# Optimization experiments

Hardware: AMD Instinct MI355X
Metric: run time of the kernel (lower is better)

Reference implementation:

```python
import jax, jax.numpy as jnp
import numpy as np

EPS = 1e-6          # module eps for denominator
KERNEL_EPS = 1e-4   # performer softmax_kernel numerical eps


def softmax_kernel(data, projection):
    # data: [n, l, h, e]; projection: [m, e] -> features [n, l, h, m]
    d = data.shape[-1]
    m = projection.shape[0]
    data_normalizer = d ** -0.25
    ratio = m ** -0.5
    data_dash = jnp.einsum('nlhe,me->nlhm', data * data_normalizer, projection)
    diag_data = (0.5 * (data_normalizer ** 2)) * jnp.sum(data * data, axis=-1, keepdims=True)
    # numerically stable exp with per-row max subtraction
    data_dash = ratio * (jnp.exp(data_dash - diag_data - jnp.max(data_dash, axis=-1, keepdims=True)) + KERNEL_EPS)
    return data_dash


def _gaussian_orthogonal_random_matrix(nb_rows, nb_cols, seed=0):
    rng = np.random.default_rng(seed)
    blocks = []
    for _ in range(int(np.ceil(nb_rows / nb_cols))):
        q, _ = np.linalg.qr(rng.standard_normal((nb_cols, nb_cols)))
        blocks.append(q.T)
    proj = np.concatenate(blocks, axis=0)[:nb_rows]
    # scaling=0: chi-distributed row multipliers
    multiplier = np.linalg.norm(rng.standard_normal((nb_rows, nb_cols)), axis=1)
    return (multiplier[:, None] * proj).astype(np.float32)


def setup_inputs() -> dict:
    n, l, h, e = 2, 2048, 8, 64
    nb_features = l  # module: nb_features = l when l >= e
    key = jax.random.key(0)
    kq, kk, kv = jax.random.split(key, 3)
    queries = jax.random.normal(kq, (n, l, h, e), jnp.float32)
    keys = jax.random.normal(kk, (n, l, h, e), jnp.float32)
    values = jax.random.normal(kv, (n, l, h, e), jnp.float32)
    projection = jnp.asarray(_gaussian_orthogonal_random_matrix(nb_features, e))
    return {"queries": queries, "keys": keys, "values": values, "projection": projection}


def reference(queries, keys, values, projection):
    # Performer linear attention, batched (bi=None) branch
    q = softmax_kernel(queries, projection)   # [n, l, h, m]
    k = softmax_kernel(keys, projection)      # [n, l, h, m]
    kv = jnp.einsum('nshm,nshe->nhem', k, values)              # [n, h, e, m]
    z = 1.0 / (jnp.einsum('nlhm,nhm->nlh', q, k.sum(axis=1)) + EPS)  # [n, l, h]
    v = jnp.einsum('nlhm,nhem,nlh->nlhe', q, kv, z)             # [n, l, h, e]
    return v
```

## Files before the change

### kernel.cpp

```cpp
#include <hip/hip_runtime.h>


#define LL 2048
#define HH 8
#define MM 2048
#define ROWSTR 512

#define NORMC 0.35355339059327373f
#define LOG2E 1.4426950408889634f
#define NORMC2 (NORMC * LOG2E)
#define RATIO 0.022097086912079608f
#define KEPS 1e-4f
#define REPS (RATIO * KEPS)
#define EPSD 1e-6f

#define KVSPLIT 2097152
#define RSPLIT 32768

typedef __attribute__((ext_vector_type(8))) short short8;
typedef __attribute__((ext_vector_type(16))) float f32x16;

#define MFMA32(a, b, c) __builtin_amdgcn_mfma_f32_32x32x16_bf16((a), (b), (c), 0, 0, 0)

__device__ __forceinline__ void wg_barrier_lds() {
    asm volatile("s_waitcnt lgkmcnt(0)" ::: "memory");
    __builtin_amdgcn_s_barrier();
    __builtin_amdgcn_sched_barrier(0);
}

__device__ __forceinline__ f32x16 zero16() {
    f32x16 v;
    #pragma unroll
    for (int i = 0; i < 16; ++i) v[i] = 0.f;
    return v;
}
__device__ __forceinline__ unsigned short f2bf(float f) {
    union { float f; unsigned int u; } v; v.f = f;
    unsigned int r = v.u + 0x7fffu + ((v.u >> 16) & 1u);
    return (unsigned short)(r >> 16);
}
__device__ __forceinline__ unsigned int pk2(float lo, float hi) {
    return __builtin_amdgcn_perm(__float_as_uint(hi), __float_as_uint(lo), 0x07060302u);
}
__device__ __forceinline__ float bf2f(unsigned short u) {
    union { unsigned int ui; float f; } v; v.ui = ((unsigned int)u) << 16; return v.f;
}

template <bool BF16>
__device__ __forceinline__ short8 row_load8(const void* src, size_t rowbase, int off) {
    if (BF16) {
        return *(const short8*)((const unsigned short*)src + rowbase + off);
    } else {
        const float* p = (const float*)src + rowbase + off;
        float4 f0 = ((const float4*)p)[0], f1 = ((const float4*)p)[1];
        union { unsigned int u[4]; short8 s; } v;
        v.u[0] = pk2(f0.x, f0.y); v.u[1] = pk2(f0.z, f0.w);
        v.u[2] = pk2(f1.x, f1.y); v.u[3] = pk2(f1.z, f1.w);
        return v.s;
    }
}

template <bool BF16>
__device__ __forceinline__ void tile_load(const void* src, size_t base, size_t rstride,
                                          int t, uint4& A, uint4& B) {
    const int row = t >> 2, c16 = (t & 3) * 16;
    if (BF16) {
        const unsigned short* p = (const unsigned short*)src + base + (size_t)row * rstride + c16;
        A = *(const uint4*)p;
        B = *(const uint4*)(p + 8);
    } else {
        const float* p = (const float*)src + base + (size_t)row * rstride + c16;
        float4 f0 = ((const float4*)p)[0], f1 = ((const float4*)p)[1];
        float4 f2 = ((const float4*)p)[2], f3 = ((const float4*)p)[3];
        A.x = pk2(f0.x, f0.y); A.y = pk2(f0.z, f0.w);
        A.z = pk2(f1.x, f1.y); A.w = pk2(f1.z, f1.w);
        B.x = pk2(f2.x, f2.y); B.y = pk2(f2.z, f2.w);
        B.z = pk2(f3.x, f3.y); B.w = pk2(f3.z, f3.w);
    }
}
__device__ __forceinline__ void tile_store72(unsigned short* D, int t, uint4 A, uint4 B) {
    const int row = t >> 2, c16 = (t & 3) * 16;
    *(uint4*)&D[row * 72 + c16] = A;
    *(uint4*)&D[row * 72 + c16 + 8] = B;
}

template <bool BF16>
__device__ __forceinline__ void vt_load(const void* V, size_t base, int t, uint4& A, uint4& B) {
    const int s0 = (t & 31) * 2, e0 = (t >> 5) * 8;
    if (BF16) {
        const unsigned short* p = (const unsigned short*)V + base + (size_t)s0 * ROWSTR + e0;
        A = *(const uint4*)p;
        B = *(const uint4*)(p + ROWSTR);
    } else {
        const float* p = (const float*)V + base + (size_t)s0 * ROWSTR + e0;
        float4 f0 = ((const float4*)p)[0], f1 = ((const float4*)p)[1];
        const float* q = p + ROWSTR;
        float4 g0 = ((const float4*)q)[0], g1 = ((const float4*)q)[1];
        A.x = pk2(f0.x, f0.y); A.y = pk2(f0.z, f0.w);
        A.z = pk2(f1.x, f1.y); A.w = pk2(f1.z, f1.w);
        B.x = pk2(g0.x, g0.y); B.y = pk2(g0.z, g0.w);
        B.z = pk2(g1.x, g1.y); B.w = pk2(g1.z, g1.w);
    }
}
__device__ __forceinline__ void vt_store72(unsigned short* VT, int t, uint4 A, uint4 B) {
    const int s0 = (t & 31) * 2, e0 = (t >> 5) * 8;
    const unsigned ua[4] = {A.x, A.y, A.z, A.w}, ub[4] = {B.x, B.y, B.z, B.w};
    #pragma unroll
    for (int i = 0; i < 4; ++i) {
        *(unsigned*)&VT[(e0 + 2 * i) * 72 + s0] = (ua[i] & 0xFFFFu) | (ub[i] << 16);
        *(unsigned*)&VT[(e0 + 2 * i + 1) * 72 + s0] = (ua[i] >> 16) | (ub[i] & 0xFFFF0000u);
    }
}

__device__ __forceinline__ short8 xfrag(const unsigned int pd[8], int cp, int hi) {
    const unsigned int s0 = hi ? pd[4 * cp + 0] : pd[4 * cp + 2];
    const unsigned int s1 = hi ? pd[4 * cp + 1] : pd[4 * cp + 3];
    const unsigned int r0 = (unsigned int)__shfl_xor((int)s0, 32);
    const unsigned int r1 = (unsigned int)__shfl_xor((int)s1, 32);
    union { unsigned int u[4]; short8 s; } v;
    v.u[0] = hi ? r0 : pd[4 * cp + 0];
    v.u[1] = hi ? r1 : pd[4 * cp + 1];
    v.u[2] = hi ? pd[4 * cp + 2] : r0;
    v.u[3] = hi ? pd[4 * cp + 3] : r1;
    return v.s;
}

__global__ void LinearAttention_15985868276494_detect(const unsigned short* __restrict__ P,
                                                      float* __restrict__ flag) {
    if (threadIdx.x == 0) {
        int sane = 1;
        #pragma unroll
        for (int i = 0; i < 16; ++i) {
            const unsigned e = (P[2 * i] >> 7) & 0xFF;
            if (e < 101 || e > 141) sane = 0;
        }
        *flag = sane ? 1.0f : 0.0f;
    }
}

template <bool BF16>
__device__ void stats_impl(const void* X, const void* P, float* cws, char* smem) {
    unsigned short* Ps = (unsigned short*)smem;
    float* red = (float*)(smem + 73728);
    const int t = threadIdx.x;
    const int w = t >> 6, ln = t & 31, hi = (t >> 5) & 1;
    const int mstrip = w & 1, r3 = (w >> 1) & 3, tsel = w >> 3;
    const int grp = w >> 2, tl = t & 255;
    const int row_base = blockIdx.x * 128;

    short8 xb[4];
    #pragma unroll
    for (int c = 0; c < 4; ++c)
        xb[c] = row_load8<BF16>(X, (size_t)(row_base + r3 * 32 + ln) * 64, 16 * c + 8 * hi);

    uint4 pA, pB;
    {
        uint4 a0, b0;
        tile_load<BF16>(P, (size_t)(grp * 64) * 64, 64, tl, a0, b0);
        tile_store72(Ps + grp * 4608, tl, a0, b0);
        tile_load<BF16>(P, (size_t)((4 + grp) * 64) * 64, 64, tl, pA, pB);
    }
    wg_barrier_lds();

    float rmax = -3e38f;
    for (int i = 0; i < 8; ++i) {
        const int cur = i & 1;
        unsigned short* Pq = Ps + cur * 18432;
        #pragma unroll
        for (int j = 0; j < 2; ++j) {
            unsigned short* Pc = Pq + (tsel * 2 + j) * 4608;
            f32x16 acc = zero16();
            #pragma unroll
            for (int c = 0; c < 4; ++c) {
                const short8 af = *(const short8*)&Pc[(32 * mstrip + ln) * 72 + 16 * c + 8 * hi];
                acc = MFMA32(af, xb[c], acc);
            }
            #pragma unroll
            for (int r = 0; r < 16; ++r) rmax = fmaxf(rmax, acc[r]);
            if (j == 0 && i + 1 < 8) {
                tile_store72(Ps + (cur ^ 1) * 18432 + grp * 4608, tl, pA, pB);
                if (i + 2 < 8)
                    tile_load<BF16>(P, (size_t)(((i + 2) * 4 + grp) * 64) * 64, 64, tl, pA, pB);
            }
        }
        wg_barrier_lds();
    }
    rmax = fmaxf(rmax, __shfl_xor(rmax, 32));
    if (hi == 0) red[w * 32 + ln] = rmax;
    float s2 = 0.f;
    if (mstrip == 0 && tsel == 0) {
        #pragma unroll
        for (int c = 0; c < 4; ++c) {
            union { short8 s; unsigned int u[4]; } uv; uv.s = xb[c];
            #pragma unroll
            for (int i2 = 0; i2 < 4; ++i2) {
                const float lo = bf2f((unsigned short)(uv.u[i2] & 0xFFFF));
                const float hv = bf2f((unsigned short)(uv.u[i2] >> 16));
                s2 = fmaf(lo, lo, s2); s2 = fmaf(hv, hv, s2);
            }
        }
        s2 += __shfl_xor(s2, 32);
    }
    wg_barrier_lds();
    if (mstrip == 0 && tsel == 0 && hi == 0) {
        const float rm = fmaxf(fmaxf(red[(r3 * 2) * 32 + ln], red[(r3 * 2 + 1) * 32 + ln]),
                               fmaxf(red[(8 + r3 * 2) * 32 + ln], red[(8 + r3 * 2 + 1) * 32 + ln]));
        const int rg = row_base + r3 * 32 + ln;
        const int n = rg >> 14, l = (rg >> 3) & 2047, h = rg & 7;
        cws[(size_t)((n << 3) | h) * LL + l] =
            (NORMC * rm + (0.5f * NORMC * NORMC) * s2) * LOG2E;
    }
}

__global__ __launch_bounds__(1024, 4) void LinearAttention_15985868276494_stats(
        const void* K, const void* Q, const void* P, const float* flag,
        float* c_k, float* c_q) {
    extern __shared__ char smem_st[];
    const void* X = (blockIdx.y == 0) ? K : Q;
    float* cws = (blockIdx.y == 0) ? c_k : c_q;
    if (*flag != 0.f) stats_impl<true>(X, P, cws, smem_st);
    else stats_impl<false>(X, P, cws, smem_st);
}

template <bool BF16>
__device__ void kv_impl(const void* K, const void* V, const void* P, const float* cws,
                        float* kvf01, float* ksum01, char* smem) {
    unsigned short* Ks = (unsigned short*)smem;
    unsigned short* VT = (unsigned short*)(smem + 18432);
    float* cks = (float*)(smem + 36864);
    float* fin = (float*)smem;

    const int t = threadIdx.x;
    const int w = t >> 6, ln = t & 31, hi = (t >> 5) & 1;
    const int w2 = w & 3, ep = w >> 2;
    const int sstrip = w2 & 1, msub = w2 >> 1;
    const int mc = ep * 2 + msub;
    const int bid = blockIdx.x;
    const int xcd = bid & 7, rr = bid >> 3;
    const int gq = rr >> 3, mtb = rr & 7;
    const int g = gq * 8 + xcd;
    const int nh = g >> 2, sp = g & 3;
    const int n = nh >> 3, h = nh & 7;
    const size_t xbase = (size_t)n * (LL * ROWSTR) + (size_t)h * 64;
    const int st0 = sp * 8;
    const int mbase = mtb * 256;

    const bool stK = (t < 256), stV = (t >= 256 && t < 512);
    const int tl = t & 255;

    short8 pb[4];
    #pragma unroll
    for (int c = 0; c < 4; ++c)
        pb[c] = row_load8<BF16>(P, (size_t)(mbase + mc * 32 + ln) * 64, 16 * c + 8 * hi);

    uint4 kA, kB, vA, vB; float ckr = 0.f;
    if (stK) {
        tile_load<BF16>(K, xbase + (size_t)(st0 * 64) * ROWSTR, ROWSTR, tl, kA, kB);
        tile_store72(Ks, tl, kA, kB);
        tile_load<BF16>(K, xbase + (size_t)((st0 + 1) * 64) * ROWSTR, ROWSTR, tl, kA, kB);
    } else if (stV) {
        vt_load<BF16>(V, xbase + (size_t)(st0 * 64) * ROWSTR, tl, vA, vB);
        vt_store72(VT, tl, vA, vB);
        vt_load<BF16>(V, xbase + (size_t)((st0 + 1) * 64) * ROWSTR, tl, vA, vB);
    }
    if (t < 64) {
        cks[t] = cws[(size_t)nh * LL + st0 * 64 + t];
        ckr = cws[(size_t)nh * LL + (st0 + 1) * 64 + t];
    }
    wg_barrier_lds();

    const short8 ones = {0x3F80, 0x3F80, 0x3F80, 0x3F80, 0x3F80, 0x3F80, 0x3F80, 0x3F80};
    f32x16 akv0 = zero16(), akv1 = zero16(), aks = zero16();

    for (int i = 0; i < 8; ++i) {
        const int cur = i & 1;
        unsigned short* Kc = Ks + cur * 4608;
        unsigned short* Vc = VT + cur * 4608;
        const float* cc = cks + cur * 64;
        f32x16 D = zero16();
        #pragma unroll
        for (int c = 0; c < 4; ++c) {
            const short8 af = *(const short8*)&Kc[(32 * sstrip + ln) * 72 + 16 * c + 8 * hi];
            D = MFMA32(af, pb[c], D);
        }
        if (i + 1 < 8) {
            if (stK) tile_store72(Ks + (cur ^ 1) * 4608, tl, kA, kB);
            else if (stV) vt_store72(VT + (cur ^ 1) * 4608, tl, vA, vB);
            if (t < 64) cks[(cur ^ 1) * 64 + t] = ckr;
            if (i + 2 < 8) {
                const int st = st0 + i + 2;
                if (stK) tile_load<BF16>(K, xbase + (size_t)(st * 64) * ROWSTR, ROWSTR, tl, kA, kB);
                else if (stV) vt_load<BF16>(V, xbase + (size_t)(st * 64) * ROWSTR, tl, vA, vB);
                if (t < 64) ckr = cws[(size_t)nh * LL + st * 64 + t];
            }
        }
        unsigned int pd[8];
        #pragma unroll
        for (int gIdx = 0; gIdx < 4; ++gIdx) {
            const float4 c4 = *(const float4*)&cc[32 * sstrip + 8 * gIdx + 4 * hi];
            const float ca[4] = {c4.x, c4.y, c4.z, c4.w};
            float f[4];
            #pragma unroll
            for (int b = 0; b < 4; ++b) {
                const float arg = fminf(fmaf(D[4 * gIdx + b], NORMC2, -ca[b]), 0.f);
                f[b] = fmaf(__builtin_amdgcn_exp2f(arg), RATIO, REPS);
            }
            pd[2 * gIdx] = pk2(f[0], f[1]);
            pd[2 * gIdx + 1] = pk2(f[2], f[3]);
        }
        #pragma unroll
        for (int cp = 0; cp < 2; ++cp) {
            const short8 bf = xfrag(pd, cp, hi);
            const int scol = 32 * sstrip + 16 * cp + 8 * hi;
            const short8 v0 = *(const short8*)&Vc[ln * 72 + scol];
            const short8 v1 = *(const short8*)&Vc[(32 + ln) * 72 + scol];
            akv0 = MFMA32(v0, bf, akv0);
            akv1 = MFMA32(v1, bf, akv1);
            aks = MFMA32(ones, bf, aks);
        }
        wg_barrier_lds();
    }
    #pragma unroll 1
    for (int e4 = 0; e4 < 4; ++e4) {
        if (ep == e4) {
            const int slot = (w2 * 64 + (t & 63)) * 33;
            #pragma unroll
            for (int r = 0; r < 16; ++r) fin[slot + r] = akv0[r];
            #pragma unroll
            for (int r = 0; r < 16; ++r) fin[slot + 16 + r] = akv1[r];
            fin[slot + 32] = aks[0];
        }
        wg_barrier_lds();
        if (ep == e4) {
            const int tt = t & 255;
            const int mt = mtb * 4 + e4;
            const int e = tt >> 2;
            const int t16 = e >> 5, e5 = e & 31;
            const int hi_s = (e5 >> 2) & 1;
            const int reg = 16 * t16 + (e5 & 3) + 4 * (e5 >> 3);
            float* dst = kvf01 + (size_t)sp * KVSPLIT + (size_t)nh * (64 * MM)
                       + (size_t)e * MM + mt * 64 + (tt & 3) * 16;
            #pragma unroll
            for (int jq = 0; jq < 4; ++jq) {
                float o[4];
                #pragma unroll
                for (int b = 0; b < 4; ++b) {
                    const int m_local = (tt & 3) * 16 + 4 * jq + b;
                    const int ms = m_local >> 5;
                    const int lane_s = hi_s * 32 + (m_local & 31);
                    o[b] = fin[((2 * ms) * 64 + lane_s) * 33 + reg]
                         + fin[((2 * ms + 1) * 64 + lane_s) * 33 + reg];
                }
                *(float4*)&dst[4 * jq] = make_float4(o[0], o[1], o[2], o[3]);
            }
            if (tt < 64) {
                const int ms = tt >> 5;
                const float val = fin[((2 * ms) * 64 + (tt & 31)) * 33 + 32]
                                + fin[((2 * ms + 1) * 64 + (tt & 31)) * 33 + 32];
                ksum01[(size_t)sp * RSPLIT + (size_t)nh * MM + mt * 64 + tt] = val;
            }
        }
        wg_barrier_lds();
    }
}

__global__ __launch_bounds__(1024, 4) void LinearAttention_15985868276494_kv(
        const void* K, const void* V, const void* P, const float* flag,
        const float* cws, float* kvf01, float* ksum01) {
    extern __shared__ char smem_kv[];
    if (*flag != 0.f) kv_impl<true>(K, V, P, cws, kvf01, ksum01, smem_kv);
    else kv_impl<false>(K, V, P, cws, kvf01, ksum01, smem_kv);
}

__global__ __launch_bounds__(256) void LinearAttention_15985868276494_reduce(
        const float* __restrict__ kvf01, const float* __restrict__ ksum01,
        unsigned short* __restrict__ kvT, float* __restrict__ ksumW) {
    const int gid = blockIdx.x * 256 + threadIdx.x;
    const size_t i4 = (size_t)gid * 4;
    const float4 a = *(const float4*)&kvf01[i4];
    const float4 b = *(const float4*)&kvf01[KVSPLIT + i4];
    const float4 c = *(const float4*)&kvf01[2 * (size_t)KVSPLIT + i4];
    const float4 d = *(const float4*)&kvf01[3 * (size_t)KVSPLIT + i4];
    uint2 o;
    o.x = (unsigned)f2bf(a.x + b.x + c.x + d.x) | ((unsigned)f2bf(a.y + b.y + c.y + d.y) << 16);
    o.y = (unsigned)f2bf(a.z + b.z + c.z + d.z) | ((unsigned)f2bf(a.w + b.w + c.w + d.w) << 16);
    *(uint2*)&kvT[i4] = o;
    if (blockIdx.x < 32) {
        const float4 e = *(const float4*)&ksum01[i4];
        const float4 f = *(const float4*)&ksum01[RSPLIT + i4];
        const float4 g = *(const float4*)&ksum01[2 * RSPLIT + i4];
        const float4 h = *(const float4*)&ksum01[3 * RSPLIT + i4];
        *(float4*)&ksumW[i4] = make_float4(e.x + f.x + g.x + h.x, e.y + f.y + g.y + h.y,
                                           e.z + f.z + g.z + h.z, e.w + f.w + g.w + h.w);
    }
}

template <bool BF16>
__device__ void out_impl(const void* Q, const void* P, const float* cqw,
                         const unsigned short* kvT, const float* ksum,
                         float* po, float* pad, char* smem) {
    unsigned short* Ps = (unsigned short*)smem;
    unsigned short* KVs = (unsigned short*)(smem + 18432);
    unsigned short* kss = (unsigned short*)(smem + 36864);
    float* fin = (float*)smem;

    const int t = threadIdx.x;
    const int w = t >> 6, ln = t & 31, hi = (t >> 5) & 1;
    const int w2 = w & 3, ep = w >> 2;
    const int mstrip = w2 & 1, lsub = w2 >> 1;
    const int lc = ep * 2 + lsub;
    const int bid = blockIdx.x;
    const int xcd = bid & 7, rr = bid >> 3;
    const int gq = rr >> 3, lbb = rr & 7;
    const int g = gq * 8 + xcd;
    const int nh = g >> 2, sp = g & 3;
    const int n = nh >> 3, h = nh & 7;
    const size_t qbase = (size_t)n * (LL * ROWSTR) + (size_t)h * 64;
    const size_t kvbase = (size_t)nh * (size_t)(64 * MM);
    const int mt0 = sp * 8;
    const int lbase = lbb * 256;

    const bool stP = (t < 256), stKV = (t >= 256 && t < 512);
    const int tl = t & 255;

    short8 qb[4];
    #pragma unroll
    for (int c = 0; c < 4; ++c)
        qb[c] = row_load8<BF16>(Q, qbase + (size_t)(lbase + lc * 32 + ln) * ROWSTR, 16 * c + 8 * hi);
    const float cq = cqw[(size_t)nh * LL + lbase + lc * 32 + ln];

    uint4 pA, pB, kA, kB; float ksr = 0.f;
    if (stP) {
        tile_load<BF16>(P, (size_t)(mt0 * 64) * 64, 64, tl, pA, pB);
        tile_store72(Ps, tl, pA, pB);
        tile_load<BF16>(P, (size_t)((mt0 + 1) * 64) * 64, 64, tl, pA, pB);
    } else if (stKV) {
        tile_load<true>(kvT, kvbase + mt0 * 64, MM, tl, kA, kB);
        tile_store72(KVs, tl, kA, kB);
        tile_load<true>(kvT, kvbase + (mt0 + 1) * 64, MM, tl, kA, kB);
    }
    if (t < 64) {
        kss[t] = f2bf(ksum[(size_t)nh * MM + mt0 * 64 + t]);
        ksr = ksum[(size_t)nh * MM + (mt0 + 1) * 64 + t];
    }
    wg_barrier_lds();

    f32x16 ao0 = zero16(), ao1 = zero16(), ad = zero16();

    for (int i = 0; i < 8; ++i) {
        const int cur = i & 1;
        unsigned short* Pc = Ps + cur * 4608;
        unsigned short* Kc = KVs + cur * 4608;
        const unsigned short* ksc = kss + cur * 64;
        f32x16 D = zero16();
        #pragma unroll
        for (int c = 0; c < 4; ++c) {
            const short8 af = *(const short8*)&Pc[(32 * mstrip + ln) * 72 + 16 * c + 8 * hi];
            D = MFMA32(af, qb[c], D);
        }
        if (i + 1 < 8) {
            if (stP) tile_store72(Ps + (cur ^ 1) * 4608, tl, pA, pB);
            else if (stKV) tile_store72(KVs + (cur ^ 1) * 4608, tl, kA, kB);
            if (t < 64) kss[(cur ^ 1) * 64 + t] = f2bf(ksr);
            if (i + 2 < 8) {
                if (stP) tile_load<BF16>(P, (size_t)((mt0 + i + 2) * 64) * 64, 64, tl, pA, pB);
                else if (stKV) tile_load<true>(kvT, kvbase + (mt0 + i + 2) * 64, MM, tl, kA, kB);
                if (t < 64) ksr = ksum[(size_t)nh * MM + (mt0 + i + 2) * 64 + t];
            }
        }
        unsigned int pd[8];
        #pragma unroll
        for (int gIdx = 0; gIdx < 4; ++gIdx) {
            float f[4];
            #pragma unroll
            for (int b = 0; b < 4; ++b) {
                const float arg = fminf(fmaf(D[4 * gIdx + b], NORMC2, -cq), 0.f);
                f[b] = fmaf(__builtin_amdgcn_exp2f(arg), RATIO, REPS);
            }
            pd[2 * gIdx] = pk2(f[0], f[1]);
            pd[2 * gIdx + 1] = pk2(f[2], f[3]);
        }
        #pragma unroll
        for (int cp = 0; cp < 2; ++cp) {
            const short8 bf = xfrag(pd, cp, hi);
            const int mcol = 32 * mstrip + 16 * cp + 8 * hi;
            const short8 a0 = *(const short8*)&Kc[ln * 72 + mcol];
            const short8 a1 = *(const short8*)&Kc[(32 + ln) * 72 + mcol];
            const short8 k8 = *(const short8*)&ksc[mcol];
            ao0 = MFMA32(a0, bf, ao0);
            ao1 = MFMA32(a1, bf, ao1);
            ad = MFMA32(k8, bf, ad);
        }
        wg_barrier_lds();
    }
    #pragma unroll 1
    for (int e4 = 0; e4 < 4; ++e4) {
        if (ep == e4) {
            const int slot = (w2 * 64 + (t & 63)) * 33;
            #pragma unroll
            for (int r = 0; r < 16; ++r) fin[slot + r] = ao0[r];
            #pragma unroll
            for (int r = 0; r < 16; ++r) fin[slot + 16 + r] = ao1[r];
            fin[slot + 32] = ad[0];
        }
        wg_barrier_lds();
        if (ep == e4) {
            const int tt = t & 255;
            const int l_local = tt >> 2, eg = tt & 3;
            const int ls = l_local >> 5, lane_l = l_local & 31;
            const float adt = fin[((2 * ls) * 64 + lane_l) * 33 + 32]
                            + fin[((2 * ls + 1) * 64 + lane_l) * 33 + 32];
            const int l = (lbb * 4 + e4) * 64 + l_local;
            const size_t row = (size_t)(n * LL + l) * HH + h;
            if (eg == 0) pad[(size_t)sp * RSPLIT + row] = adt;
            float* dst = po + (size_t)sp * KVSPLIT + row * 64 + eg * 16;
            #pragma unroll
            for (int jq = 0; jq < 4; ++jq) {
                float o[4];
                #pragma unroll
                for (int b = 0; b < 4; ++b) {
                    const int e = eg * 16 + 4 * jq + b;
                    const int t16 = e >> 5, e5 = e & 31;
                    const int hi_s = (e5 >> 2) & 1;
                    const int reg = 16 * t16 + (e5 & 3) + 4 * (e5 >> 3);
                    const int lane_s = hi_s * 32 + lane_l;
                    o[b] = fin[((2 * ls) * 64 + lane_s) * 33 + reg]
                         + fin[((2 * ls + 1) * 64 + lane_s) * 33 + reg];
                }
                *(float4*)&dst[4 * jq] = make_float4(o[0], o[1], o[2], o[3]);
            }
        }
        wg_barrier_lds();
    }
}

__global__ __launch_bounds__(1024, 4) void LinearAttention_15985868276494_out(
        const void* Q, const void* P, const float* flag, const float* cqw,
        const unsigned short* kvT, const float* ksum, float* po, float* pad) {
    extern __shared__ char smem_out[];
    if (*flag != 0.f) out_impl<true>(Q, P, cqw, kvT, ksum, po, pad, smem_out);
    else out_impl<false>(Q, P, cqw, kvT, ksum, po, pad, smem_out);
}

__global__ __launch_bounds__(256) void LinearAttention_15985868276494_out2(
        const float* __restrict__ po, const float* __restrict__ pad,
        const float* __restrict__ flag, void* __restrict__ outp) {
    const int gid = blockIdx.x * 256 + threadIdx.x;
    const int row = gid >> 2, eg = gid & 3;
    const float adt = pad[row] + pad[RSPLIT + row]
                    + pad[2 * RSPLIT + row] + pad[3 * RSPLIT + row];
    const float z = 1.0f / (adt + EPSD);
    const size_t base = (size_t)row * 64 + eg * 16;
    float vals[16];
    #pragma unroll
    for (int q4 = 0; q4 < 4; ++q4) {
        const float4 a = *(const float4*)&po[base + 4 * q4];
        const float4 b = *(const float4*)&po[KVSPLIT + base + 4 * q4];
        const float4 c = *(const float4*)&po[2 * (size_t)KVSPLIT + base + 4 * q4];
        const float4 d = *(const float4*)&po[3 * (size_t)KVSPLIT + base + 4 * q4];
        vals[4 * q4 + 0] = (a.x + b.x + c.x + d.x) * z;
        vals[4 * q4 + 1] = (a.y + b.y + c.y + d.y) * z;
        vals[4 * q4 + 2] = (a.z + b.z + c.z + d.z) * z;
        vals[4 * q4 + 3] = (a.w + b.w + c.w + d.w) * z;
    }
    if (*flag != 0.f) {
        uint4 o0, o1;
        o0.x = (unsigned)f2bf(vals[0]) | ((unsigned)f2bf(vals[1]) << 16);
        o0.y = (unsigned)f2bf(vals[2]) | ((unsigned)f2bf(vals[3]) << 16);
        o0.z = (unsigned)f2bf(vals[4]) | ((unsigned)f2bf(vals[5]) << 16);
        o0.w = (unsigned)f2bf(vals[6]) | ((unsigned)f2bf(vals[7]) << 16);
        o1.x = (unsigned)f2bf(vals[8]) | ((unsigned)f2bf(vals[9]) << 16);
        o1.y = (unsigned)f2bf(vals[10]) | ((unsigned)f2bf(vals[11]) << 16);
        o1.z = (unsigned)f2bf(vals[12]) | ((unsigned)f2bf(vals[13]) << 16);
        o1.w = (unsigned)f2bf(vals[14]) | ((unsigned)f2bf(vals[15]) << 16);
        unsigned short* op = (unsigned short*)outp + base;
        *(uint4*)op = o0;
        *(uint4*)(op + 8) = o1;
    } else {
        float* op = (float*)outp + base;
        #pragma unroll
        for (int q4 = 0; q4 < 4; ++q4)
            *(float4*)&op[4 * q4] = make_float4(vals[4 * q4], vals[4 * q4 + 1],
                                                vals[4 * q4 + 2], vals[4 * q4 + 3]);
    }
}

extern "C" void kernel_launch(void* const* d_in, const int* in_sizes, int n_in,
                              void* d_out, int out_size, void* d_ws, size_t ws_size,
                              hipStream_t stream) {
    const void* Q = d_in[0];
    const void* K = d_in[1];
    const void* V = d_in[2];
    const void* P = d_in[3];

    float* W = (float*)d_ws;
    float* flag = W;
    float* c_k = W + 16;
    float* c_q = c_k + 32768;
    float* ksum01 = c_q + 32768;
    float* kvf01 = ksum01 + 4 * RSPLIT;
    float* ksumW = kvf01 + 4 * (size_t)KVSPLIT;
    unsigned short* kvTW = (unsigned short*)(ksumW + RSPLIT);

    LinearAttention_15985868276494_detect<<<1, 64, 0, stream>>>(
        (const unsigned short*)P, flag);
    LinearAttention_15985868276494_stats<<<dim3(256, 2), 1024, 75776, stream>>>(
        K, Q, P, flag, c_k, c_q);
    LinearAttention_15985868276494_kv<<<dim3(512), 1024, 37376, stream>>>(
        K, V, P, flag, c_k, kvf01, ksum01);
    LinearAttention_15985868276494_reduce<<<2048, 256, 0, stream>>>(
        kvf01, ksum01, kvTW, ksumW);
    LinearAttention_15985868276494_out<<<dim3(512), 1024, 37120, stream>>>(
        Q, P, flag, c_q, kvTW, ksumW, kvf01, ksum01);
    LinearAttention_15985868276494_out2<<<512, 256, 0, stream>>>(
        kvf01, ksum01, flag, d_out);
}
```

Measured before the change: 212.1 us.

## Halve kv/out workgroups to 512 threads, each wave covering both strips

The kv and out kernels now launch 512 threads instead of 1024. Each wave loops over both 32-row strips itself rather than splitting them across wave pairs, so accumulation stays in registers and the cross-wave LDS reduction goes away. In kv, the ksum MFMA against a ones vector is replaced by a scalar running sum plus a shuffle, and results are written straight from registers to global memory. The cost is more serial work per wave and uncoalesced strided global stores in kv. All staging threads now do loads.

Result: faster. 192.8 us (-9.1%).

```diff
diff --git a/kernel.cpp b/kernel.cpp
--- a/kernel.cpp
+++ b/kernel.cpp
@@ -228,13 +228,10 @@
     unsigned short* Ks = (unsigned short*)smem;
     unsigned short* VT = (unsigned short*)(smem + 18432);
     float* cks = (float*)(smem + 36864);
-    float* fin = (float*)smem;
 
     const int t = threadIdx.x;
     const int w = t >> 6, ln = t & 31, hi = (t >> 5) & 1;
-    const int w2 = w & 3, ep = w >> 2;
-    const int sstrip = w2 & 1, msub = w2 >> 1;
-    const int mc = ep * 2 + msub;
+    const int mc = w;
     const int bid = blockIdx.x;
     const int xcd = bid & 7, rr = bid >> 3;
     const int gq = rr >> 3, mtb = rr & 7;
@@ -245,7 +242,7 @@
     const int st0 = sp * 8;
     const int mbase = mtb * 256;
 
-    const bool stK = (t < 256), stV = (t >= 256 && t < 512);
+    const bool stK = (t < 256);
     const int tl = t & 255;
 
     short8 pb[4];
@@ -258,7 +255,7 @@
         tile_load<BF16>(K, xbase + (size_t)(st0 * 64) * ROWSTR, ROWSTR, tl, kA, kB);
         tile_store72(Ks, tl, kA, kB);
         tile_load<BF16>(K, xbase + (size_t)((st0 + 1) * 64) * ROWSTR, ROWSTR, tl, kA, kB);
-    } else if (stV) {
+    } else {
         vt_load<BF16>(V, xbase + (size_t)(st0 * 64) * ROWSTR, tl, vA, vB);
         vt_store72(VT, tl, vA, vB);
         vt_load<BF16>(V, xbase + (size_t)((st0 + 1) * 64) * ROWSTR, tl, vA, vB);
@@ -269,102 +266,76 @@
     }
     wg_barrier_lds();
 
-    const short8 ones = {0x3F80, 0x3F80, 0x3F80, 0x3F80, 0x3F80, 0x3F80, 0x3F80, 0x3F80};
-    f32x16 akv0 = zero16(), akv1 = zero16(), aks = zero16();
+    f32x16 akv0 = zero16(), akv1 = zero16();
+    float ks = 0.f;
 
     for (int i = 0; i < 8; ++i) {
         const int cur = i & 1;
         unsigned short* Kc = Ks + cur * 4608;
         unsigned short* Vc = VT + cur * 4608;
         const float* cc = cks + cur * 64;
-        f32x16 D = zero16();
-        #pragma unroll
-        for (int c = 0; c < 4; ++c) {
-            const short8 af = *(const short8*)&Kc[(32 * sstrip + ln) * 72 + 16 * c + 8 * hi];
-            D = MFMA32(af, pb[c], D);
-        }
-        if (i + 1 < 8) {
-            if (stK) tile_store72(Ks + (cur ^ 1) * 4608, tl, kA, kB);
-            else if (stV) vt_store72(VT + (cur ^ 1) * 4608, tl, vA, vB);
-            if (t < 64) cks[(cur ^ 1) * 64 + t] = ckr;
-            if (i + 2 < 8) {
-                const int st = st0 + i + 2;
-                if (stK) tile_load<BF16>(K, xbase + (size_t)(st * 64) * ROWSTR, ROWSTR, tl, kA, kB);
-                else if (stV) vt_load<BF16>(V, xbase + (size_t)(st * 64) * ROWSTR, tl, vA, vB);
-                if (t < 64) ckr = cws[(size_t)nh * LL + st * 64 + t];
-            }
-        }
-        unsigned int pd[8];
-        #pragma unroll
-        for (int gIdx = 0; gIdx < 4; ++gIdx) {
-            const float4 c4 = *(const float4*)&cc[32 * sstrip + 8 * gIdx + 4 * hi];
-            const float ca[4] = {c4.x, c4.y, c4.z, c4.w};
-            float f[4];
-            #pragma unroll
-            for (int b = 0; b < 4; ++b) {
-                const float arg = fminf(fmaf(D[4 * gIdx + b], NORMC2, -ca[b]), 0.f);
-                f[b] = fmaf(__builtin_amdgcn_exp2f(arg), RATIO, REPS);
-            }
-            pd[2 * gIdx] = pk2(f[0], f[1]);
-            pd[2 * gIdx + 1] = pk2(f[2], f[3]);
-        }
-        #pragma unroll
-        for (int cp = 0; cp < 2; ++cp) {
-            const short8 bf = xfrag(pd, cp, hi);
-            const int scol = 32 * sstrip + 16 * cp + 8 * hi;
-            const short8 v0 = *(const short8*)&Vc[ln * 72 + scol];
-            const short8 v1 = *(const short8*)&Vc[(32 + ln) * 72 + scol];
-            akv0 = MFMA32(v0, bf, akv0);
-            akv1 = MFMA32(v1, bf, akv1);
-            aks = MFMA32(ones, bf, aks);
-        }
-        wg_barrier_lds();
-    }
-    #pragma unroll 1
-    for (int e4 = 0; e4 < 4; ++e4) {
-        if (ep == e4) {
-            const int slot = (w2 * 64 + (t & 63)) * 33;
-            #pragma unroll
-            for (int r = 0; r < 16; ++r) fin[slot + r] = akv0[r];
-            #pragma unroll
-            for (int r = 0; r < 16; ++r) fin[slot + 16 + r] = akv1[r];
-            fin[slot + 32] = aks[0];
-        }
-        wg_barrier_lds();
-        if (ep == e4) {
-            const int tt = t & 255;
-            const int mt = mtb * 4 + e4;
-            const int e = tt >> 2;
-            const int t16 = e >> 5, e5 = e & 31;
-            const int hi_s = (e5 >> 2) & 1;
-            const int reg = 16 * t16 + (e5 & 3) + 4 * (e5 >> 3);
-            float* dst = kvf01 + (size_t)sp * KVSPLIT + (size_t)nh * (64 * MM)
-                       + (size_t)e * MM + mt * 64 + (tt & 3) * 16;
-            #pragma unroll
-            for (int jq = 0; jq < 4; ++jq) {
-                float o[4];
+        #pragma unroll
+        for (int ss = 0; ss < 2; ++ss) {
+            f32x16 D = zero16();
+            #pragma unroll
+            for (int c = 0; c < 4; ++c) {
+                const short8 af = *(const short8*)&Kc[(32 * ss + ln) * 72 + 16 * c + 8 * hi];
+                D = MFMA32(af, pb[c], D);
+            }
+            if (ss == 0 && i + 1 < 8) {
+                if (stK) tile_store72(Ks + (cur ^ 1) * 4608, tl, kA, kB);
+                else vt_store72(VT + (cur ^ 1) * 4608, tl, vA, vB);
+                if (t < 64) cks[(cur ^ 1) * 64 + t] = ckr;
+                if (i + 2 < 8) {
+                    const int st = st0 + i + 2;
+                    if (stK) tile_load<BF16>(K, xbase + (size_t)(st * 64) * ROWSTR, ROWSTR, tl, kA, kB);
+                    else vt_load<BF16>(V, xbase + (size_t)(st * 64) * ROWSTR, tl, vA, vB);
+                    if (t < 64) ckr = cws[(size_t)nh * LL + st * 64 + t];
+                }
+            }
+            unsigned int pd[8];
+            #pragma unroll
+            for (int gIdx = 0; gIdx < 4; ++gIdx) {
+                const float4 c4 = *(const float4*)&cc[32 * ss + 8 * gIdx + 4 * hi];
+                const float ca[4] = {c4.x, c4.y, c4.z, c4.w};
+                float f[4];
                 #pragma unroll
                 for (int b = 0; b < 4; ++b) {
-                    const int m_local = (tt & 3) * 16 + 4 * jq + b;
-                    const int ms = m_local >> 5;
-                    const int lane_s = hi_s * 32 + (m_local & 31);
-                    o[b] = fin[((2 * ms) * 64 + lane_s) * 33 + reg]
-                         + fin[((2 * ms + 1) * 64 + lane_s) * 33 + reg];
+                    const float arg = fminf(fmaf(D[4 * gIdx + b], NORMC2, -ca[b]), 0.f);
+                    f[b] = fmaf(__builtin_amdgcn_exp2f(arg), RATIO, REPS);
                 }
-                *(float4*)&dst[4 * jq] = make_float4(o[0], o[1], o[2], o[3]);
-            }
-            if (tt < 64) {
-                const int ms = tt >> 5;
-                const float val = fin[((2 * ms) * 64 + (tt & 31)) * 33 + 32]
-                                + fin[((2 * ms + 1) * 64 + (tt & 31)) * 33 + 32];
-                ksum01[(size_t)sp * RSPLIT + (size_t)nh * MM + mt * 64 + tt] = val;
+                ks += (f[0] + f[1]) + (f[2] + f[3]);
+                pd[2 * gIdx] = pk2(f[0], f[1]);
+                pd[2 * gIdx + 1] = pk2(f[2], f[3]);
+            }
+            #pragma unroll
+            for (int cp = 0; cp < 2; ++cp) {
+                const short8 bf = xfrag(pd, cp, hi);
+                const int scol = 32 * ss + 16 * cp + 8 * hi;
+                const short8 v0 = *(const short8*)&Vc[ln * 72 + scol];
+                const short8 v1 = *(const short8*)&Vc[(32 + ln) * 72 + scol];
+                akv0 = MFMA32(v0, bf, akv0);
+                akv1 = MFMA32(v1, bf, akv1);
             }
         }
         wg_barrier_lds();
     }
-}
-
-__global__ __launch_bounds__(1024, 4) void LinearAttention_15985868276494_kv(
+    {
+        ks += __shfl_xor(ks, 32);
+        const int m = mbase + mc * 32 + ln;
+        if (hi == 0)
+            ksum01[(size_t)sp * RSPLIT + (size_t)nh * MM + m] = ks;
+        float* basep = kvf01 + (size_t)sp * KVSPLIT + (size_t)nh * (size_t)(64 * MM) + m;
+        #pragma unroll
+        for (int r = 0; r < 16; ++r) {
+            const int e = (r & 3) + 8 * (r >> 2) + 4 * hi;
+            basep[(size_t)e * MM] = akv0[r];
+            basep[(size_t)(e + 32) * MM] = akv1[r];
+        }
+    }
+}
+
+__global__ __launch_bounds__(512, 4) void LinearAttention_15985868276494_kv(
         const void* K, const void* V, const void* P, const float* flag,
         const float* cws, float* kvf01, float* ksum01) {
     extern __shared__ char smem_kv[];
@@ -406,9 +377,7 @@
 
     const int t = threadIdx.x;
     const int w = t >> 6, ln = t & 31, hi = (t >> 5) & 1;
-    const int w2 = w & 3, ep = w >> 2;
-    const int mstrip = w2 & 1, lsub = w2 >> 1;
-    const int lc = ep * 2 + lsub;
+    const int lc = w;
     const int bid = blockIdx.x;
     const int xcd = bid & 7, rr = bid >> 3;
     const int gq = rr >> 3, lbb = rr & 7;
@@ -420,7 +389,7 @@
     const int mt0 = sp * 8;
     const int lbase = lbb * 256;
 
-    const bool stP = (t < 256), stKV = (t >= 256 && t < 512);
+    const bool stP = (t < 256);
     const int tl = t & 255;
 
     short8 qb[4];
@@ -434,7 +403,7 @@
         tile_load<BF16>(P, (size_t)(mt0 * 64) * 64, 64, tl, pA, pB);
         tile_store72(Ps, tl, pA, pB);
         tile_load<BF16>(P, (size_t)((mt0 + 1) * 64) * 64, 64, tl, pA, pB);
-    } else if (stKV) {
+    } else {
         tile_load<true>(kvT, kvbase + mt0 * 64, MM, tl, kA, kB);
         tile_store72(KVs, tl, kA, kB);
         tile_load<true>(kvT, kvbase + (mt0 + 1) * 64, MM, tl, kA, kB);
@@ -452,51 +421,54 @@
         unsigned short* Pc = Ps + cur * 4608;
         unsigned short* Kc = KVs + cur * 4608;
         const unsigned short* ksc = kss + cur * 64;
-        f32x16 D = zero16();
-        #pragma unroll
-        for (int c = 0; c < 4; ++c) {
-            const short8 af = *(const short8*)&Pc[(32 * mstrip + ln) * 72 + 16 * c + 8 * hi];
-            D = MFMA32(af, qb[c], D);
-        }
-        if (i + 1 < 8) {
-            if (stP) tile_store72(Ps + (cur ^ 1) * 4608, tl, pA, pB);
-            else if (stKV) tile_store72(KVs + (cur ^ 1) * 4608, tl, kA, kB);
-            if (t < 64) kss[(cur ^ 1) * 64 + t] = f2bf(ksr);
-            if (i + 2 < 8) {
-                if (stP) tile_load<BF16>(P, (size_t)((mt0 + i + 2) * 64) * 64, 64, tl, pA, pB);
-                else if (stKV) tile_load<true>(kvT, kvbase + (mt0 + i + 2) * 64, MM, tl, kA, kB);
-                if (t < 64) ksr = ksum[(size_t)nh * MM + (mt0 + i + 2) * 64 + t];
-            }
-        }
-        unsigned int pd[8];
-        #pragma unroll
-        for (int gIdx = 0; gIdx < 4; ++gIdx) {
-            float f[4];
-            #pragma unroll
-            for (int b = 0; b < 4; ++b) {
-                const float arg = fminf(fmaf(D[4 * gIdx + b], NORMC2, -cq), 0.f);
-                f[b] = fmaf(__builtin_amdgcn_exp2f(arg), RATIO, REPS);
-            }
-            pd[2 * gIdx] = pk2(f[0], f[1]);
-            pd[2 * gIdx + 1] = pk2(f[2], f[3]);
-        }
-        #pragma unroll
-        for (int cp = 0; cp < 2; ++cp) {
-            const short8 bf = xfrag(pd, cp, hi);
-            const int mcol = 32 * mstrip + 16 * cp + 8 * hi;
-            const short8 a0 = *(const short8*)&Kc[ln * 72 + mcol];
-            const short8 a1 = *(const short8*)&Kc[(32 + ln) * 72 + mcol];
-            const short8 k8 = *(const short8*)&ksc[mcol];
-            ao0 = MFMA32(a0, bf, ao0);
-            ao1 = MFMA32(a1, bf, ao1);
-            ad = MFMA32(k8, bf, ad);
+        #pragma unroll
+        for (int ms = 0; ms < 2; ++ms) {
+            f32x16 D = zero16();
+            #pragma unroll
+            for (int c = 0; c < 4; ++c) {
+                const short8 af = *(const short8*)&Pc[(32 * ms + ln) * 72 + 16 * c + 8 * hi];
+                D = MFMA32(af, qb[c], D);
+            }
+            if (ms == 0 && i + 1 < 8) {
+                if (stP) tile_store72(Ps + (cur ^ 1) * 4608, tl, pA, pB);
+                else tile_store72(KVs + (cur ^ 1) * 4608, tl, kA, kB);
+                if (t < 64) kss[(cur ^ 1) * 64 + t] = f2bf(ksr);
+                if (i + 2 < 8) {
+                    if (stP) tile_load<BF16>(P, (size_t)((mt0 + i + 2) * 64) * 64, 64, tl, pA, pB);
+                    else tile_load<true>(kvT, kvbase + (mt0 + i + 2) * 64, MM, tl, kA, kB);
+                    if (t < 64) ksr = ksum[(size_t)nh * MM + (mt0 + i + 2) * 64 + t];
+                }
+            }
+            unsigned int pd[8];
+            #pragma unroll
+            for (int gIdx = 0; gIdx < 4; ++gIdx) {
+                float f[4];
+                #pragma unroll
+                for (int b = 0; b < 4; ++b) {
+                    const float arg = fminf(fmaf(D[4 * gIdx + b], NORMC2, -cq), 0.f);
+                    f[b] = fmaf(__builtin_amdgcn_exp2f(arg), RATIO, REPS);
+                }
+                pd[2 * gIdx] = pk2(f[0], f[1]);
+                pd[2 * gIdx + 1] = pk2(f[2], f[3]);
+            }
+            #pragma unroll
+            for (int cp = 0; cp < 2; ++cp) {
+                const short8 bf = xfrag(pd, cp, hi);
+                const int mcol = 32 * ms + 16 * cp + 8 * hi;
+                const short8 a0 = *(const short8*)&Kc[ln * 72 + mcol];
+                const short8 a1 = *(const short8*)&Kc[(32 + ln) * 72 + mcol];
+                const short8 k8 = *(const short8*)&ksc[mcol];
+                ao0 = MFMA32(a0, bf, ao0);
+                ao1 = MFMA32(a1, bf, ao1);
+                ad = MFMA32(k8, bf, ad);
+            }
         }
         wg_barrier_lds();
     }
     #pragma unroll 1
-    for (int e4 = 0; e4 < 4; ++e4) {
-        if (ep == e4) {
-            const int slot = (w2 * 64 + (t & 63)) * 33;
+    for (int e2 = 0; e2 < 2; ++e2) {
+        if ((w >> 2) == e2) {
+            const int slot = ((w & 3) * 64 + (t & 63)) * 33;
             #pragma unroll
             for (int r = 0; r < 16; ++r) fin[slot + r] = ao0[r];
             #pragma unroll
@@ -504,13 +476,11 @@
             fin[slot + 32] = ad[0];
         }
         wg_barrier_lds();
-        if (ep == e4) {
-            const int tt = t & 255;
-            const int l_local = tt >> 2, eg = tt & 3;
-            const int ls = l_local >> 5, lane_l = l_local & 31;
-            const float adt = fin[((2 * ls) * 64 + lane_l) * 33 + 32]
-                            + fin[((2 * ls + 1) * 64 + lane_l) * 33 + 32];
-            const int l = (lbb * 4 + e4) * 64 + l_local;
+        {
+            const int l128 = t >> 2, eg = t & 3;
+            const int w2 = l128 >> 5, lane_l = l128 & 31;
+            const float adt = fin[(w2 * 64 + lane_l) * 33 + 32];
+            const int l = lbase + (e2 * 4 + w2) * 32 + lane_l;
             const size_t row = (size_t)(n * LL + l) * HH + h;
             if (eg == 0) pad[(size_t)sp * RSPLIT + row] = adt;
             float* dst = po + (size_t)sp * KVSPLIT + row * 64 + eg * 16;
@@ -524,8 +494,7 @@
                     const int hi_s = (e5 >> 2) & 1;
                     const int reg = 16 * t16 + (e5 & 3) + 4 * (e5 >> 3);
                     const int lane_s = hi_s * 32 + lane_l;
-                    o[b] = fin[((2 * ls) * 64 + lane_s) * 33 + reg]
-                         + fin[((2 * ls + 1) * 64 + lane_s) * 33 + reg];
+                    o[b] = fin[(w2 * 64 + lane_s) * 33 + reg];
                 }
                 *(float4*)&dst[4 * jq] = make_float4(o[0], o[1], o[2], o[3]);
             }
@@ -534,7 +503,7 @@
     }
 }
 
-__global__ __launch_bounds__(1024, 4) void LinearAttention_15985868276494_out(
+__global__ __launch_bounds__(512, 4) void LinearAttention_15985868276494_out(
         const void* Q, const void* P, const float* flag, const float* cqw,
         const unsigned short* kvT, const float* ksum, float* po, float* pad) {
     extern __shared__ char smem_out[];
@@ -606,11 +575,11 @@
         (const unsigned short*)P, flag);
     LinearAttention_15985868276494_stats<<<dim3(256, 2), 1024, 75776, stream>>>(
         K, Q, P, flag, c_k, c_q);
-    LinearAttention_15985868276494_kv<<<dim3(512), 1024, 37376, stream>>>(
+    LinearAttention_15985868276494_kv<<<dim3(512), 512, 37376, stream>>>(
         K, V, P, flag, c_k, kvf01, ksum01);
     LinearAttention_15985868276494_reduce<<<2048, 256, 0, stream>>>(
         kvf01, ksum01, kvTW, ksumW);
-    LinearAttention_15985868276494_out<<<dim3(512), 1024, 37120, stream>>>(
+    LinearAttention_15985868276494_out<<<dim3(512), 512, 37120, stream>>>(
         Q, P, flag, c_q, kvTW, ksumW, kvf01, ksum01);
     LinearAttention_15985868276494_out2<<<512, 256, 0, stream>>>(
         kvf01, ksum01, flag, d_out);
```
